# Performance work log

Measured on AMD Instinct MI355X. Metric: run time of the kernel, lower is better.

Reference implementation:

```python
import jax, jax.numpy as jnp
import numpy as np

EPS = 1e-5
HALT_THRESHOLD = 0.01
DILATIONS = (1, 2, 4)


def layer_norm(x, g, b):
    m = jnp.mean(x, axis=-1, keepdims=True)
    v = jnp.var(x, axis=-1, keepdims=True)
    return (x - m) * jax.lax.rsqrt(v + EPS) * g + b


def depthwise_conv(x, k, dilation):
    # x: [B,H,W,C], k: [kh,kw,1,C] (groups == C)
    pad = dilation * (k.shape[0] // 2)
    return jax.lax.conv_general_dilated(
        x, k, window_strides=(1, 1), padding=[(pad, pad), (pad, pad)],
        rhs_dilation=(dilation, dilation),
        dimension_numbers=('NHWC', 'HWIO', 'NHWC'),
        feature_group_count=x.shape[-1])


def setup_inputs() -> dict:
    key = jax.random.key(0)
    ks = jax.random.split(key, 12)
    B, H, W, C = 8, 96, 96, 64
    hid = 64
    P = C + len(DILATIONS) * C  # 256
    n = jax.random.normal
    return {
        'x': n(ks[0], (B, H, W, C), dtype=jnp.float32),
        'g1': jnp.ones((C,), jnp.float32), 'b1': jnp.zeros((C,), jnp.float32),
        'g2': jnp.ones((P,), jnp.float32), 'b2': jnp.zeros((P,), jnp.float32),
        'k1': 0.2 * n(ks[1], (3, 3, 1, C), dtype=jnp.float32),
        'k2': 0.2 * n(ks[2], (3, 3, 1, C), dtype=jnp.float32),
        'k3': 0.2 * n(ks[3], (3, 3, 1, C), dtype=jnp.float32),
        'Wu1': n(ks[4], (P, 2 * hid), dtype=jnp.float32) / np.sqrt(P),
        'bu1': jnp.zeros((2 * hid,), jnp.float32),
        'Wu2': n(ks[5], (2 * hid, hid), dtype=jnp.float32) / np.sqrt(2 * hid),
        'bu2': jnp.zeros((hid,), jnp.float32),
        'Wu3': n(ks[6], (hid, C), dtype=jnp.float32) / np.sqrt(hid),
        'bu3': jnp.zeros((C,), jnp.float32),
        'gh': jnp.ones((C,), jnp.float32), 'bh': jnp.zeros((C,), jnp.float32),
        'Wh1': n(ks[7], (C, hid), dtype=jnp.float32) / np.sqrt(C),
        'bh1': jnp.zeros((hid,), jnp.float32),
        'Wh2': n(ks[8], (hid, 1), dtype=jnp.float32) / np.sqrt(hid),
        'bh2': jnp.zeros((1,), jnp.float32),
        'max_steps': 8, 'min_steps': 1,
    }


def reference(x, g1, b1, g2, b2, k1, k2, k3, Wu1, bu1, Wu2, bu2, Wu3, bu3,
              gh, bh, Wh1, bh1, Wh2, bh2, max_steps, min_steps):
    gelu = lambda t: jax.nn.gelu(t, approximate=False)

    def forward_step(xs):
        # halt unit: LN -> Linear -> GELU -> Linear -> sigmoid
        h = gelu(layer_norm(xs, gh, bh) @ Wh1 + bh1)
        halt_probs = jax.nn.sigmoid(h @ Wh2 + bh2)[..., 0]  # [B,H,W]
        xn = layer_norm(xs, g1, b1)
        ps = [depthwise_conv(xn, k, d) for k, d in zip((k1, k2, k3), DILATIONS)]
        u = layer_norm(jnp.concatenate([xn] + ps, axis=-1), g2, b2)
        h1 = gelu(u @ Wu1 + bu1)
        h2 = gelu(h1 @ Wu2 + bu2)
        delta = h2 @ Wu3 + bu3
        return delta, halt_probs

    B, H, W, C = x.shape
    halted0 = jnp.zeros((B, H, W), jnp.bool_)
    acc0 = jnp.zeros((B, H, W), x.dtype)
    so0 = jnp.zeros_like(x)
    pc0 = jnp.zeros((B, H, W), x.dtype)

    def body(carry, step):
        xs, halted, acc, so, pc = carry
        delta, hp = forward_step(xs)
        active = ~halted
        af = active.astype(xs.dtype)
        xs = xs + delta * af[..., None]
        in_halt_phase = step >= (min_steps - 1)
        acc_n = acc + hp * af
        should_halt = (acc_n > 1.0 - HALT_THRESHOLD) & active
        halt_w = jnp.where(should_halt, 1.0 - (acc_n - hp), hp * af)
        so_n = so + xs * halt_w[..., None]
        halted_n = halted | should_halt
        acc = jnp.where(in_halt_phase, acc_n, acc)
        so = jnp.where(in_halt_phase, so_n, so)
        halted = jnp.where(in_halt_phase, halted_n, halted)
        pc = pc + jnp.where(in_halt_phase, af, jnp.ones_like(pc))
        return (xs, halted, acc, so, pc), None

    (xf, halted, acc, so, pc), _ = jax.lax.scan(
        body, (x, halted0, acc0, so0, pc0), jnp.arange(max_steps))
    # distribute remaining probability mass to cells that never halted
    remaining_w = (~halted).astype(x.dtype) * (1.0 - acc)
    so = so + xf * remaining_w[..., None]
    pc = pc / max_steps
    return so, halted, pc
```

## Files before the change

kernel.cpp:

```cpp
#include <hip/hip_runtime.h>
#include <hip/hip_bf16.h>

#define NPIX 73728
#define CH 64
#define HH 96
#define WW 96
#define PP 256

typedef __attribute__((ext_vector_type(8))) short short8;
typedef __attribute__((ext_vector_type(4))) float f32x4;

__device__ __forceinline__ float wsum64(float v) {
#pragma unroll
  for (int off = 32; off > 0; off >>= 1) v += __shfl_xor(v, off, 64);
  return v;
}
__device__ __forceinline__ float wsum16(float v) {
#pragma unroll
  for (int off = 1; off < 16; off <<= 1) v += __shfl_xor(v, off, 64);
  return v;
}
__device__ __forceinline__ float gelu_f(float x) {
  return 0.5f * x * (1.0f + erff(x * 0.70710678118654752f));
}
__device__ __forceinline__ float b2f(ushort u) {
  union { unsigned int i; float f; } c;
  c.i = ((unsigned int)u) << 16;
  return c.f;
}
__device__ __forceinline__ ushort f2b(float f) {
  union { float f; unsigned int i; } c;
  c.f = f;
  unsigned int r = c.i + 0x7fff + ((c.i >> 16) & 1);
  return (ushort)(r >> 16);
}

__global__ __launch_bounds__(256) void k_init(const float* __restrict__ x,
                                              float* __restrict__ xs,
                                              float* __restrict__ out,
                                              float* __restrict__ accb,
                                              float* __restrict__ xnf,
                                              int* __restrict__ cnt) {
  int i = blockIdx.x * 256 + threadIdx.x;
  if (i < NPIX * CH) xs[i] = x[i];
  if (i < NPIX * 66) out[i] = 0.0f;
  if (i < NPIX) { accb[i] = 0.0f; xnf[i] = 0.0f; }
  if (i < 8) cnt[i] = 0;
}

__global__ __launch_bounds__(256) void k_wprep(const float* __restrict__ W,
                                               ushort* __restrict__ Wp, int K,
                                               int N) {
  int t = blockIdx.x * 256 + threadIdx.x;
  if (t >= K * N) return;
  int j = t & 7, l = (t >> 3) & 63, tile = t >> 9;
  int NT = N >> 4;
  int kt = tile / NT, nt = tile - kt * NT;
  int k = kt * 32 + ((l >> 4) & 3) * 8 + j;
  int n = nt * 16 + (l & 15);
  Wp[t] = f2b(W[k * N + n]);
}

__global__ __launch_bounds__(256) void k_compact(const float* __restrict__ halted,
                                                 int* __restrict__ cnt,
                                                 int* __restrict__ idx, int step) {
  int p = blockIdx.x * 256 + threadIdx.x;
  bool active = (halted[p] == 0.0f);
  unsigned long long mask = __ballot(active);
  int lane = threadIdx.x & 63;
  int cw = __popcll(mask);
  int wbase = 0;
  if (lane == 0 && cw) wbase = atomicAdd(&cnt[step], cw);
  wbase = __shfl(wbase, 0, 64);
  if (active) {
    int off = __popcll(mask & ((1ull << lane) - 1ull));
    idx[wbase + off] = p;
  }
}

__global__ __launch_bounds__(256) void k_ln_halt(
    const float* __restrict__ xs, ushort* __restrict__ xn, float* __restrict__ hp,
    const float* __restrict__ halted, float* __restrict__ xnf,
    const float* __restrict__ g1, const float* __restrict__ b1,
    const float* __restrict__ gh, const float* __restrict__ bh,
    const float* __restrict__ Wh1, const float* __restrict__ bh1,
    const float* __restrict__ Wh2, const float* __restrict__ bh2) {
  __shared__ float lnbuf[4][64];
  __shared__ float partials[4][4][64];
  __shared__ int actf[4];
  int wave = threadIdx.x >> 6, lane = threadIdx.x & 63;
  int pix = blockIdx.x * 4 + wave;
  float hf = halted[pix];
  bool act = !(hf != 0.0f && xnf[pix] != 0.0f);
  if (lane == 0) actf[wave] = act ? 1 : 0;
  if (act) {
    float x = xs[(size_t)pix * CH + lane];
    float mean = wsum64(x) * (1.0f / 64.0f);
    float d = x - mean;
    float var = wsum64(d * d) * (1.0f / 64.0f);
    float rstd = rsqrtf(var + 1e-5f);
    float nrm = d * rstd;
    xn[(size_t)pix * CH + lane] = f2b(nrm * g1[lane] + b1[lane]);
    lnbuf[wave][lane] = nrm * gh[lane] + bh[lane];
    if (lane == 0) xnf[pix] = hf;
  } else {
    lnbuf[wave][lane] = 0.0f;
  }
  __syncthreads();
  if (!(actf[0] | actf[1] | actf[2] | actf[3])) return;

  float start = (wave == 0) ? bh1[lane] : 0.0f;
  float p0 = start, p1 = start, p2 = start, p3 = start;
  int i0 = wave * 16;
#pragma unroll 4
  for (int i = i0; i < i0 + 16; ++i) {
    float w = Wh1[i * 64 + lane];
    p0 = fmaf(lnbuf[0][i], w, p0);
    p1 = fmaf(lnbuf[1][i], w, p1);
    p2 = fmaf(lnbuf[2][i], w, p2);
    p3 = fmaf(lnbuf[3][i], w, p3);
  }
  partials[wave][0][lane] = p0;
  partials[wave][1][lane] = p1;
  partials[wave][2][lane] = p2;
  partials[wave][3][lane] = p3;
  __syncthreads();

  if (actf[wave]) {
    float s = (partials[0][wave][lane] + partials[1][wave][lane]) +
              (partials[2][wave][lane] + partials[3][wave][lane]);
    float acc = gelu_f(s);
    float c = wsum64(acc * Wh2[lane]);
    if (lane == 0) hp[pix] = 1.0f / (1.0f + expf(-(c + bh2[0])));
  }
}

template <bool EDGE>
__device__ __forceinline__ void do_taps(const ushort* pb,
                                        const float* __restrict__ k1,
                                        const float* __restrict__ k2,
                                        const float* __restrict__ k3, int cg,
                                        int y, int xq, float (&br)[4][4]) {
#pragma unroll
  for (int t = 0; t < 3; ++t) {
    const int dl = (t == 0) ? 1 : ((t == 1) ? 2 : 4);
    const float* kk = (t == 0) ? k1 : ((t == 1) ? k2 : k3);
    float a0 = 0.f, a1 = 0.f, a2 = 0.f, a3 = 0.f;
#pragma unroll
    for (int ky = 0; ky < 3; ++ky) {
#pragma unroll
      for (int kx = 0; kx < 3; ++kx) {
        const int dy = (ky - 1) * dl, dx = (kx - 1) * dl;
        if (EDGE && !(ky == 1 && kx == 1)) {
          if ((unsigned)(y + dy) >= HH) continue;
        }
        const float4 w = *(const float4*)&kk[(ky * 3 + kx) * CH + cg * 4];
        float v0, v1, v2, v3;
        if (ky == 1 && kx == 1) {
          v0 = br[0][0]; v1 = br[0][1]; v2 = br[0][2]; v3 = br[0][3];
        } else {
          ushort4 d4 = *(const ushort4*)(pb + (dy * WW + dx) * CH);
          v0 = b2f(d4.x); v1 = b2f(d4.y); v2 = b2f(d4.z); v3 = b2f(d4.w);
          if (EDGE && (unsigned)(xq + dx) >= WW) {
            v0 = 0.f; v1 = 0.f; v2 = 0.f; v3 = 0.f;
          }
        }
        a0 = fmaf(v0, w.x, a0); a1 = fmaf(v1, w.y, a1);
        a2 = fmaf(v2, w.z, a2); a3 = fmaf(v3, w.w, a3);
      }
    }
    br[t + 1][0] = a0; br[t + 1][1] = a1;
    br[t + 1][2] = a2; br[t + 1][3] = a3;
  }
}

__global__ __launch_bounds__(256) void k_conv_u(
    const ushort* __restrict__ xn, ushort* __restrict__ u,
    const int* __restrict__ idx, const int* __restrict__ cnt, int step,
    const float* __restrict__ k1, const float* __restrict__ k2,
    const float* __restrict__ k3, const float* __restrict__ g2,
    const float* __restrict__ b2) {
  int n = cnt[step];
  if (blockIdx.x * 16 >= n) return;
  int wv = threadIdx.x >> 6, l = threadIdx.x & 63;
  int cpx = l >> 4, cg = l & 15;
  int slot = blockIdx.x * 16 + wv * 4 + cpx;
  bool live = slot < n;
  int pix = idx[live ? slot : (n - 1)];
  int b = pix / (HH * WW);
  int rem = pix - b * (HH * WW);
  int y = rem / WW, xq = rem - (rem / WW) * WW;
  const ushort* pb = xn + (size_t)pix * CH + cg * 4;

  float br[4][4];
  {
    ushort4 c4 = *(const ushort4*)pb;
    br[0][0] = b2f(c4.x); br[0][1] = b2f(c4.y);
    br[0][2] = b2f(c4.z); br[0][3] = b2f(c4.w);
  }
  bool interior = (xq >= 4) && (xq <= WW - 5) && (y >= 4) && (y <= HH - 5);
  if (__all(interior))
    do_taps<false>(pb, k1, k2, k3, cg, y, xq, br);
  else
    do_taps<true>(pb, k1, k2, k3, cg, y, xq, br);

  float s = 0.f;
#pragma unroll
  for (int t = 0; t < 4; ++t)
#pragma unroll
    for (int c = 0; c < 4; ++c) s += br[t][c];
  float mean = wsum16(s) * (1.0f / 256.0f);
  float vs = 0.f;
#pragma unroll
  for (int t = 0; t < 4; ++t)
#pragma unroll
    for (int c = 0; c < 4; ++c) {
      float d = br[t][c] - mean;
      vs += d * d;
    }
  float rstd = rsqrtf(wsum16(vs) * (1.0f / 256.0f) + 1e-5f);
  ushort* ub = u + (size_t)blockIdx.x * 4096;
  int lr16 = wv * 4 + cpx;
  if (live) {
#pragma unroll
    for (int t = 0; t < 4; ++t) {
      float4 g = *(const float4*)&g2[t * CH + cg * 4];
      float4 bb = *(const float4*)&b2[t * CH + cg * 4];
      ushort4 o;
      o.x = f2b((br[t][0] - mean) * rstd * g.x + bb.x);
      o.y = f2b((br[t][1] - mean) * rstd * g.y + bb.y);
      o.z = f2b((br[t][2] - mean) * rstd * g.z + bb.z);
      o.w = f2b((br[t][3] - mean) * rstd * g.w + bb.w);
      int k0 = t * 64 + cg * 4;
      int kt = k0 >> 5, lg = (k0 >> 3) & 3, jj = k0 & 7;
      *(ushort4*)(ub + kt * 512 + (lg * 16 + lr16) * 8 + jj) = o;
    }
  }
}

__global__ __launch_bounds__(64) void k_mlp(
    const ushort* __restrict__ u, const int* __restrict__ idx,
    const int* __restrict__ cnt, int step, const ushort* __restrict__ Wp1,
    const ushort* __restrict__ Wp2, const ushort* __restrict__ Wp3,
    const float* __restrict__ bu1, const float* __restrict__ bu2,
    const float* __restrict__ bu3, const float* __restrict__ hp,
    float* __restrict__ xs, float* __restrict__ so, float* __restrict__ halted,
    float* __restrict__ accb, float* __restrict__ pc,
    const int* __restrict__ min_steps) {
  int n = cnt[step];
  if (blockIdx.x * 16 >= n) return;
  __shared__ ushort h1s[16 * 136];
  __shared__ ushort h2s[16 * 72];
  int l = threadIdx.x;
  int lr = l & 15, lg = l >> 4;
  const f32x4 vzero = {0.0f, 0.0f, 0.0f, 0.0f};

  int msteps = min_steps[0];
  bool in_halt = (step >= msteps - 1);
  int px = l >> 2, q = l & 3;
  int slotp = blockIdx.x * 16 + px;
  bool livep = slotp < n;
  int p = idx[livep ? slotp : (n - 1)];
  size_t base = (size_t)p * CH + q * 16;
  float4 xv[4], sv[4];
#pragma unroll
  for (int j = 0; j < 4; ++j) xv[j] = *(const float4*)&xs[base + j * 4];
  if (in_halt) {
#pragma unroll
    for (int j = 0; j < 4; ++j) sv[j] = *(const float4*)&so[base + j * 4];
  }
  float hpv = hp[p];
  float accv = accb[p];

  const ushort* ub = u + (size_t)blockIdx.x * 4096 + l * 8;
  short8 a[8];
#pragma unroll
  for (int kt = 0; kt < 8; ++kt) a[kt] = *(const short8*)(ub + kt * 512);
  f32x4 acc1[8];
#pragma unroll
  for (int nt = 0; nt < 8; ++nt) acc1[nt] = vzero;
#pragma unroll
  for (int kt = 0; kt < 8; ++kt) {
#pragma unroll
    for (int nt = 0; nt < 8; ++nt) {
      short8 b = *(const short8*)(Wp1 + ((kt * 8 + nt) * 64 + l) * 8);
      acc1[nt] = __builtin_amdgcn_mfma_f32_16x16x32_bf16(a[kt], b, acc1[nt], 0, 0, 0);
    }
  }
  ushort* h1w = h1s;
#pragma unroll
  for (int nt = 0; nt < 8; ++nt) {
    float bb = bu1[nt * 16 + lr];
#pragma unroll
    for (int i = 0; i < 4; ++i)
      h1w[(lg * 4 + i) * 136 + nt * 16 + lr] = f2b(gelu_f(acc1[nt][i] + bb));
  }

  f32x4 acc2[4];
#pragma unroll
  for (int nt = 0; nt < 4; ++nt) acc2[nt] = vzero;
#pragma unroll
  for (int kt = 0; kt < 4; ++kt) {
    short8 av = *(const short8*)(h1w + lr * 136 + kt * 32 + lg * 8);
#pragma unroll
    for (int nt = 0; nt < 4; ++nt) {
      short8 b = *(const short8*)(Wp2 + ((kt * 4 + nt) * 64 + l) * 8);
      acc2[nt] = __builtin_amdgcn_mfma_f32_16x16x32_bf16(av, b, acc2[nt], 0, 0, 0);
    }
  }
  ushort* h2w = h2s;
#pragma unroll
  for (int nt = 0; nt < 4; ++nt) {
    float bb = bu2[nt * 16 + lr];
#pragma unroll
    for (int i = 0; i < 4; ++i)
      h2w[(lg * 4 + i) * 72 + nt * 16 + lr] = f2b(gelu_f(acc2[nt][i] + bb));
  }

  f32x4 acc3[4];
#pragma unroll
  for (int nt = 0; nt < 4; ++nt) acc3[nt] = vzero;
#pragma unroll
  for (int kt = 0; kt < 2; ++kt) {
    short8 av = *(const short8*)(h2w + lr * 72 + kt * 32 + lg * 8);
#pragma unroll
    for (int nt = 0; nt < 4; ++nt) {
      short8 b = *(const short8*)(Wp3 + ((kt * 4 + nt) * 64 + l) * 8);
      acc3[nt] = __builtin_amdgcn_mfma_f32_16x16x32_bf16(av, b, acc3[nt], 0, 0, 0);
    }
  }
  float* df = (float*)h1w;
#pragma unroll
  for (int nt = 0; nt < 4; ++nt) {
    float bb = bu3[nt * 16 + lr];
#pragma unroll
    for (int i = 0; i < 4; ++i)
      df[(lg * 4 + i) * 68 + nt * 16 + lr] = acc3[nt][i] + bb;
  }

  if (livep) {
    float acc_n = accv + hpv;
    bool should_halt = (acc_n > 0.99f);
    float halt_w = should_halt ? (1.0f - (acc_n - hpv)) : hpv;
#pragma unroll
    for (int j = 0; j < 4; ++j) {
      float4 dv = *(const float4*)&df[px * 68 + q * 16 + j * 4];
      float4 x2 = xv[j];
      x2.x += dv.x; x2.y += dv.y; x2.z += dv.z; x2.w += dv.w;
      *(float4*)&xs[base + j * 4] = x2;
      if (in_halt) {
        float4 s2 = sv[j];
        s2.x += x2.x * halt_w;
        s2.y += x2.y * halt_w;
        s2.z += x2.z * halt_w;
        s2.w += x2.w * halt_w;
        *(float4*)&so[base + j * 4] = s2;
      }
    }
    if (q == 0) {
      if (in_halt) {
        accb[p] = acc_n;
        halted[p] = should_halt ? 1.0f : 0.0f;
      }
      pc[p] += 1.0f;
    }
  }
}

__global__ __launch_bounds__(256) void k_final(
    const float* __restrict__ xs, float* __restrict__ so,
    const float* __restrict__ halted, const float* __restrict__ accb,
    float* __restrict__ pc, const int* __restrict__ max_steps) {
  int wave = threadIdx.x >> 6, lane = threadIdx.x & 63;
  int pix = blockIdx.x * 4 + wave;
  float rem = (halted[pix] == 0.0f) ? (1.0f - accb[pix]) : 0.0f;
  so[(size_t)pix * CH + lane] += xs[(size_t)pix * CH + lane] * rem;
  if (lane == 0) pc[pix] *= 1.0f / (float)max_steps[0];
}

extern "C" void kernel_launch(void* const* d_in, const int* in_sizes, int n_in,
                              void* d_out, int out_size, void* d_ws,
                              size_t ws_size, hipStream_t stream) {
  const float* x   = (const float*)d_in[0];
  const float* g1  = (const float*)d_in[1];
  const float* b1  = (const float*)d_in[2];
  const float* g2  = (const float*)d_in[3];
  const float* b2  = (const float*)d_in[4];
  const float* k1  = (const float*)d_in[5];
  const float* k2  = (const float*)d_in[6];
  const float* k3  = (const float*)d_in[7];
  const float* Wu1 = (const float*)d_in[8];
  const float* bu1 = (const float*)d_in[9];
  const float* Wu2 = (const float*)d_in[10];
  const float* bu2 = (const float*)d_in[11];
  const float* Wu3 = (const float*)d_in[12];
  const float* bu3 = (const float*)d_in[13];
  const float* gh  = (const float*)d_in[14];
  const float* bh  = (const float*)d_in[15];
  const float* Wh1 = (const float*)d_in[16];
  const float* bh1 = (const float*)d_in[17];
  const float* Wh2 = (const float*)d_in[18];
  const float* bh2 = (const float*)d_in[19];
  const int* max_steps = (const int*)d_in[20];
  const int* min_steps = (const int*)d_in[21];

  if (ws_size < (size_t)68000000) return;
  char* ws = (char*)d_ws;
  float*  xs   = (float*)(ws);
  ushort* xn   = (ushort*)(ws + 18874368);
  ushort* u    = (ushort*)(ws + 28311552);
  float*  hp   = (float*)(ws + 66060288);
  float*  accb = (float*)(ws + 66355200);
  ushort* Wp1  = (ushort*)(ws + 66650112);
  ushort* Wp2  = (ushort*)(ws + 66715648);
  ushort* Wp3  = (ushort*)(ws + 66732032);
  float*  xnf  = (float*)(ws + 66740224);
  int*    idx  = (int*)(ws + 67035136);
  int*    cnt  = (int*)(ws + 67330048);
  float* so = (float*)d_out;
  float* halted = so + (size_t)NPIX * CH;
  float* pc = halted + NPIX;

  k_wprep<<<128, 256, 0, stream>>>(Wu1, Wp1, 256, 128);
  k_wprep<<<32, 256, 0, stream>>>(Wu2, Wp2, 128, 64);
  k_wprep<<<16, 256, 0, stream>>>(Wu3, Wp3, 64, 64);
  k_init<<<19008, 256, 0, stream>>>(x, xs, so, accb, xnf, cnt);
  for (int step = 0; step < 8; ++step) {
    k_compact<<<NPIX / 256, 256, 0, stream>>>(halted, cnt, idx, step);
    k_ln_halt<<<NPIX / 4, 256, 0, stream>>>(xs, xn, hp, halted, xnf, g1, b1,
                                            gh, bh, Wh1, bh1, Wh2, bh2);
    k_conv_u<<<NPIX / 16, 256, 0, stream>>>(xn, u, idx, cnt, step, k1, k2, k3,
                                            g2, b2);
    k_mlp<<<NPIX / 16, 64, 0, stream>>>(u, idx, cnt, step, Wp1, Wp2, Wp3, bu1,
                                        bu2, bu3, hp, xs, so, halted, accb, pc,
                                        min_steps);
  }
  k_final<<<NPIX / 4, 256, 0, stream>>>(xs, so, halted, accb, pc, max_steps);
}
```

Before: 694.1 us.

## Fuse depthwise conv and LayerNorm into the MLP kernel via an LDS slab

Removes the separate conv+LN kernel and computes the dilated depthwise convolutions and the 256-channel LayerNorm inside the MLP kernel. The result goes straight into a shared-memory slab in MFMA operand layout instead of a global `u` buffer. This drops a large global write and read of the bf16 intermediate, plus one launch per step. In exchange, each 64-thread block now does the conv work serially over four iterations instead of using four waves, which lengthens per-block latency and raises register and LDS use.

```diff
diff --git a/kernel.cpp b/kernel.cpp
--- a/kernel.cpp
+++ b/kernel.cpp
@@ -174,81 +174,21 @@
   }
 }
 
-__global__ __launch_bounds__(256) void k_conv_u(
-    const ushort* __restrict__ xn, ushort* __restrict__ u,
-    const int* __restrict__ idx, const int* __restrict__ cnt, int step,
-    const float* __restrict__ k1, const float* __restrict__ k2,
-    const float* __restrict__ k3, const float* __restrict__ g2,
-    const float* __restrict__ b2) {
-  int n = cnt[step];
-  if (blockIdx.x * 16 >= n) return;
-  int wv = threadIdx.x >> 6, l = threadIdx.x & 63;
-  int cpx = l >> 4, cg = l & 15;
-  int slot = blockIdx.x * 16 + wv * 4 + cpx;
-  bool live = slot < n;
-  int pix = idx[live ? slot : (n - 1)];
-  int b = pix / (HH * WW);
-  int rem = pix - b * (HH * WW);
-  int y = rem / WW, xq = rem - (rem / WW) * WW;
-  const ushort* pb = xn + (size_t)pix * CH + cg * 4;
-
-  float br[4][4];
-  {
-    ushort4 c4 = *(const ushort4*)pb;
-    br[0][0] = b2f(c4.x); br[0][1] = b2f(c4.y);
-    br[0][2] = b2f(c4.z); br[0][3] = b2f(c4.w);
-  }
-  bool interior = (xq >= 4) && (xq <= WW - 5) && (y >= 4) && (y <= HH - 5);
-  if (__all(interior))
-    do_taps<false>(pb, k1, k2, k3, cg, y, xq, br);
-  else
-    do_taps<true>(pb, k1, k2, k3, cg, y, xq, br);
-
-  float s = 0.f;
-#pragma unroll
-  for (int t = 0; t < 4; ++t)
-#pragma unroll
-    for (int c = 0; c < 4; ++c) s += br[t][c];
-  float mean = wsum16(s) * (1.0f / 256.0f);
-  float vs = 0.f;
-#pragma unroll
-  for (int t = 0; t < 4; ++t)
-#pragma unroll
-    for (int c = 0; c < 4; ++c) {
-      float d = br[t][c] - mean;
-      vs += d * d;
-    }
-  float rstd = rsqrtf(wsum16(vs) * (1.0f / 256.0f) + 1e-5f);
-  ushort* ub = u + (size_t)blockIdx.x * 4096;
-  int lr16 = wv * 4 + cpx;
-  if (live) {
-#pragma unroll
-    for (int t = 0; t < 4; ++t) {
-      float4 g = *(const float4*)&g2[t * CH + cg * 4];
-      float4 bb = *(const float4*)&b2[t * CH + cg * 4];
-      ushort4 o;
-      o.x = f2b((br[t][0] - mean) * rstd * g.x + bb.x);
-      o.y = f2b((br[t][1] - mean) * rstd * g.y + bb.y);
-      o.z = f2b((br[t][2] - mean) * rstd * g.z + bb.z);
-      o.w = f2b((br[t][3] - mean) * rstd * g.w + bb.w);
-      int k0 = t * 64 + cg * 4;
-      int kt = k0 >> 5, lg = (k0 >> 3) & 3, jj = k0 & 7;
-      *(ushort4*)(ub + kt * 512 + (lg * 16 + lr16) * 8 + jj) = o;
-    }
-  }
-}
-
 __global__ __launch_bounds__(64) void k_mlp(
-    const ushort* __restrict__ u, const int* __restrict__ idx,
-    const int* __restrict__ cnt, int step, const ushort* __restrict__ Wp1,
-    const ushort* __restrict__ Wp2, const ushort* __restrict__ Wp3,
-    const float* __restrict__ bu1, const float* __restrict__ bu2,
-    const float* __restrict__ bu3, const float* __restrict__ hp,
-    float* __restrict__ xs, float* __restrict__ so, float* __restrict__ halted,
+    const ushort* __restrict__ xn, const int* __restrict__ idx,
+    const int* __restrict__ cnt, int step, const float* __restrict__ k1,
+    const float* __restrict__ k2, const float* __restrict__ k3,
+    const float* __restrict__ g2, const float* __restrict__ b2,
+    const ushort* __restrict__ Wp1, const ushort* __restrict__ Wp2,
+    const ushort* __restrict__ Wp3, const float* __restrict__ bu1,
+    const float* __restrict__ bu2, const float* __restrict__ bu3,
+    const float* __restrict__ hp, float* __restrict__ xs,
+    float* __restrict__ so, float* __restrict__ halted,
     float* __restrict__ accb, float* __restrict__ pc,
     const int* __restrict__ min_steps) {
   int n = cnt[step];
   if (blockIdx.x * 16 >= n) return;
+  __shared__ ushort uslab[4096];
   __shared__ ushort h1s[16 * 136];
   __shared__ ushort h2s[16 * 72];
   int l = threadIdx.x;
@@ -272,10 +212,67 @@
   float hpv = hp[p];
   float accv = accb[p];
 
-  const ushort* ub = u + (size_t)blockIdx.x * 4096 + l * 8;
+  {
+    int cpx = l >> 4, cg = l & 15;
+#pragma unroll
+    for (int it = 0; it < 4; ++it) {
+      int slot = blockIdx.x * 16 + it * 4 + cpx;
+      bool live = slot < n;
+      int pix = idx[live ? slot : (n - 1)];
+      int b = pix / (HH * WW);
+      int rem = pix - b * (HH * WW);
+      int y = rem / WW, xq = rem - (rem / WW) * WW;
+      const ushort* pb = xn + (size_t)pix * CH + cg * 4;
+      float br[4][4];
+      {
+        ushort4 c4 = *(const ushort4*)pb;
+        br[0][0] = b2f(c4.x); br[0][1] = b2f(c4.y);
+        br[0][2] = b2f(c4.z); br[0][3] = b2f(c4.w);
+      }
+      bool interior = (xq >= 4) && (xq <= WW - 5) && (y >= 4) && (y <= HH - 5);
+      if (__all(interior))
+        do_taps<false>(pb, k1, k2, k3, cg, y, xq, br);
+      else
+        do_taps<true>(pb, k1, k2, k3, cg, y, xq, br);
+
+      float s = 0.f;
+#pragma unroll
+      for (int t = 0; t < 4; ++t)
+#pragma unroll
+        for (int c = 0; c < 4; ++c) s += br[t][c];
+      float mean = wsum16(s) * (1.0f / 256.0f);
+      float vs = 0.f;
+#pragma unroll
+      for (int t = 0; t < 4; ++t)
+#pragma unroll
+        for (int c = 0; c < 4; ++c) {
+          float d = br[t][c] - mean;
+          vs += d * d;
+        }
+      float rstd = rsqrtf(wsum16(vs) * (1.0f / 256.0f) + 1e-5f);
+      int lr16 = it * 4 + cpx;
+      if (live) {
+#pragma unroll
+        for (int t = 0; t < 4; ++t) {
+          float4 g = *(const float4*)&g2[t * CH + cg * 4];
+          float4 bb = *(const float4*)&b2[t * CH + cg * 4];
+          ushort4 o;
+          o.x = f2b((br[t][0] - mean) * rstd * g.x + bb.x);
+          o.y = f2b((br[t][1] - mean) * rstd * g.y + bb.y);
+          o.z = f2b((br[t][2] - mean) * rstd * g.z + bb.z);
+          o.w = f2b((br[t][3] - mean) * rstd * g.w + bb.w);
+          int k0 = t * 64 + cg * 4;
+          int kt = k0 >> 5, lg2 = (k0 >> 3) & 3, jj = k0 & 7;
+          *(ushort4*)(uslab + kt * 512 + (lg2 * 16 + lr16) * 8 + jj) = o;
+        }
+      }
+    }
+  }
+
   short8 a[8];
 #pragma unroll
-  for (int kt = 0; kt < 8; ++kt) a[kt] = *(const short8*)(ub + kt * 512);
+  for (int kt = 0; kt < 8; ++kt)
+    a[kt] = *(const short8*)(uslab + kt * 512 + l * 8);
   f32x4 acc1[8];
 #pragma unroll
   for (int nt = 0; nt < 8; ++nt) acc1[nt] = vzero;
@@ -408,7 +405,6 @@
   char* ws = (char*)d_ws;
   float*  xs   = (float*)(ws);
   ushort* xn   = (ushort*)(ws + 18874368);
-  ushort* u    = (ushort*)(ws + 28311552);
   float*  hp   = (float*)(ws + 66060288);
   float*  accb = (float*)(ws + 66355200);
   ushort* Wp1  = (ushort*)(ws + 66650112);
@@ -429,11 +425,9 @@
     k_compact<<<NPIX / 256, 256, 0, stream>>>(halted, cnt, idx, step);
     k_ln_halt<<<NPIX / 4, 256, 0, stream>>>(xs, xn, hp, halted, xnf, g1, b1,
                                             gh, bh, Wh1, bh1, Wh2, bh2);
-    k_conv_u<<<NPIX / 16, 256, 0, stream>>>(xn, u, idx, cnt, step, k1, k2, k3,
-                                            g2, b2);
-    k_mlp<<<NPIX / 16, 64, 0, stream>>>(u, idx, cnt, step, Wp1, Wp2, Wp3, bu1,
-                                        bu2, bu3, hp, xs, so, halted, accb, pc,
-                                        min_steps);
+    k_mlp<<<NPIX / 16, 64, 0, stream>>>(xn, idx, cnt, step, k1, k2, k3, g2, b2,
+                                        Wp1, Wp2, Wp3, bu1, bu2, bu3, hp, xs,
+                                        so, halted, accb, pc, min_steps);
   }
   k_final<<<NPIX / 4, 256, 0, stream>>>(xs, so, halted, accb, pc, max_steps);
 }
```

Result: slower. 841.3 us (+21.2%).

## Fuse active-pixel compaction into MLP kernel and drive LN/halt from compacted lists

Applied to the files above, without the earlier changes.

Removes the separate per-step compaction kernel. The MLP epilogue now appends still-active pixels to the next step's index list through a wave ballot and an atomic. The LN/halt kernel now iterates over a compacted list (the previous step's list, which still covers pixels that halted on the last step and need xn for the conv halo) instead of launching over every pixel and checking the halted and xnf flags. This saves one launch per step and the full-grid scans, but it needs per-step index storage and changes the order of pixel indices from sequential to atomic-driven, which can hurt memory locality.

```diff
diff --git a/kernel.cpp b/kernel.cpp
--- a/kernel.cpp
+++ b/kernel.cpp
@@ -39,13 +39,13 @@
                                               float* __restrict__ xs,
                                               float* __restrict__ out,
                                               float* __restrict__ accb,
-                                              float* __restrict__ xnf,
+                                              int* __restrict__ idx,
                                               int* __restrict__ cnt) {
   int i = blockIdx.x * 256 + threadIdx.x;
   if (i < NPIX * CH) xs[i] = x[i];
   if (i < NPIX * 66) out[i] = 0.0f;
-  if (i < NPIX) { accb[i] = 0.0f; xnf[i] = 0.0f; }
-  if (i < 8) cnt[i] = 0;
+  if (i < NPIX) { accb[i] = 0.0f; idx[i] = i; }
+  if (i < 9) cnt[i] = (i == 0) ? NPIX : 0;
 }
 
 __global__ __launch_bounds__(256) void k_wprep(const float* __restrict__ W,
@@ -61,38 +61,21 @@
   Wp[t] = f2b(W[k * N + n]);
 }
 
-__global__ __launch_bounds__(256) void k_compact(const float* __restrict__ halted,
-                                                 int* __restrict__ cnt,
-                                                 int* __restrict__ idx, int step) {
-  int p = blockIdx.x * 256 + threadIdx.x;
-  bool active = (halted[p] == 0.0f);
-  unsigned long long mask = __ballot(active);
-  int lane = threadIdx.x & 63;
-  int cw = __popcll(mask);
-  int wbase = 0;
-  if (lane == 0 && cw) wbase = atomicAdd(&cnt[step], cw);
-  wbase = __shfl(wbase, 0, 64);
-  if (active) {
-    int off = __popcll(mask & ((1ull << lane) - 1ull));
-    idx[wbase + off] = p;
-  }
-}
-
 __global__ __launch_bounds__(256) void k_ln_halt(
     const float* __restrict__ xs, ushort* __restrict__ xn, float* __restrict__ hp,
-    const float* __restrict__ halted, float* __restrict__ xnf,
+    const int* __restrict__ lst, const int* __restrict__ cnt, int lslot,
     const float* __restrict__ g1, const float* __restrict__ b1,
     const float* __restrict__ gh, const float* __restrict__ bh,
     const float* __restrict__ Wh1, const float* __restrict__ bh1,
     const float* __restrict__ Wh2, const float* __restrict__ bh2) {
+  int m = cnt[lslot];
+  if (blockIdx.x * 4 >= m) return;
   __shared__ float lnbuf[4][64];
   __shared__ float partials[4][4][64];
-  __shared__ int actf[4];
   int wave = threadIdx.x >> 6, lane = threadIdx.x & 63;
-  int pix = blockIdx.x * 4 + wave;
-  float hf = halted[pix];
-  bool act = !(hf != 0.0f && xnf[pix] != 0.0f);
-  if (lane == 0) actf[wave] = act ? 1 : 0;
+  int slot = blockIdx.x * 4 + wave;
+  bool act = slot < m;
+  int pix = lst[act ? slot : m - 1];
   if (act) {
     float x = xs[(size_t)pix * CH + lane];
     float mean = wsum64(x) * (1.0f / 64.0f);
@@ -102,12 +85,10 @@
     float nrm = d * rstd;
     xn[(size_t)pix * CH + lane] = f2b(nrm * g1[lane] + b1[lane]);
     lnbuf[wave][lane] = nrm * gh[lane] + bh[lane];
-    if (lane == 0) xnf[pix] = hf;
   } else {
     lnbuf[wave][lane] = 0.0f;
   }
   __syncthreads();
-  if (!(actf[0] | actf[1] | actf[2] | actf[3])) return;
 
   float start = (wave == 0) ? bh1[lane] : 0.0f;
   float p0 = start, p1 = start, p2 = start, p3 = start;
@@ -126,7 +107,7 @@
   partials[wave][3][lane] = p3;
   __syncthreads();
 
-  if (actf[wave]) {
+  if (act) {
     float s = (partials[0][wave][lane] + partials[1][wave][lane]) +
               (partials[2][wave][lane] + partials[3][wave][lane]);
     float acc = gelu_f(s);
@@ -176,7 +157,7 @@
 
 __global__ __launch_bounds__(256) void k_conv_u(
     const ushort* __restrict__ xn, ushort* __restrict__ u,
-    const int* __restrict__ idx, const int* __restrict__ cnt, int step,
+    const int* __restrict__ lst, const int* __restrict__ cnt, int step,
     const float* __restrict__ k1, const float* __restrict__ k2,
     const float* __restrict__ k3, const float* __restrict__ g2,
     const float* __restrict__ b2) {
@@ -186,7 +167,7 @@
   int cpx = l >> 4, cg = l & 15;
   int slot = blockIdx.x * 16 + wv * 4 + cpx;
   bool live = slot < n;
-  int pix = idx[live ? slot : (n - 1)];
+  int pix = lst[live ? slot : (n - 1)];
   int b = pix / (HH * WW);
   int rem = pix - b * (HH * WW);
   int y = rem / WW, xq = rem - (rem / WW) * WW;
@@ -239,12 +220,13 @@
 }
 
 __global__ __launch_bounds__(64) void k_mlp(
-    const ushort* __restrict__ u, const int* __restrict__ idx,
-    const int* __restrict__ cnt, int step, const ushort* __restrict__ Wp1,
-    const ushort* __restrict__ Wp2, const ushort* __restrict__ Wp3,
-    const float* __restrict__ bu1, const float* __restrict__ bu2,
-    const float* __restrict__ bu3, const float* __restrict__ hp,
-    float* __restrict__ xs, float* __restrict__ so, float* __restrict__ halted,
+    const ushort* __restrict__ u, const int* __restrict__ lst,
+    int* __restrict__ nxt, int* __restrict__ cnt, int step,
+    const ushort* __restrict__ Wp1, const ushort* __restrict__ Wp2,
+    const ushort* __restrict__ Wp3, const float* __restrict__ bu1,
+    const float* __restrict__ bu2, const float* __restrict__ bu3,
+    const float* __restrict__ hp, float* __restrict__ xs,
+    float* __restrict__ so, float* __restrict__ halted,
     float* __restrict__ accb, float* __restrict__ pc,
     const int* __restrict__ min_steps) {
   int n = cnt[step];
@@ -260,7 +242,7 @@
   int px = l >> 2, q = l & 3;
   int slotp = blockIdx.x * 16 + px;
   bool livep = slotp < n;
-  int p = idx[livep ? slotp : (n - 1)];
+  int p = lst[livep ? slotp : (n - 1)];
   size_t base = (size_t)p * CH + q * 16;
   float4 xv[4], sv[4];
 #pragma unroll
@@ -338,10 +320,10 @@
       df[(lg * 4 + i) * 68 + nt * 16 + lr] = acc3[nt][i] + bb;
   }
 
+  float acc_n = accv + hpv;
+  bool should_halt = in_halt && (acc_n > 0.99f);
   if (livep) {
-    float acc_n = accv + hpv;
-    bool should_halt = (acc_n > 0.99f);
-    float halt_w = should_halt ? (1.0f - (acc_n - hpv)) : hpv;
+    float halt_w = (acc_n > 0.99f) ? (1.0f - (acc_n - hpv)) : hpv;
 #pragma unroll
     for (int j = 0; j < 4; ++j) {
       float4 dv = *(const float4*)&df[px * 68 + q * 16 + j * 4];
@@ -364,6 +346,17 @@
       }
       pc[p] += 1.0f;
     }
+  }
+
+  bool keep = livep && !should_halt;
+  unsigned long long m_ = __ballot(q == 0 && keep);
+  int cw = __popcll(m_);
+  int wbase = 0;
+  if (l == 0 && cw) wbase = atomicAdd(&cnt[step + 1], cw);
+  wbase = __shfl(wbase, 0, 64);
+  if (q == 0 && keep) {
+    int off = __popcll(m_ & ((1ull << l) - 1ull));
+    nxt[wbase + off] = p;
   }
 }
 
@@ -404,7 +397,7 @@
   const int* max_steps = (const int*)d_in[20];
   const int* min_steps = (const int*)d_in[21];
 
-  if (ws_size < (size_t)68000000) return;
+  if (ws_size < (size_t)70000000) return;
   char* ws = (char*)d_ws;
   float*  xs   = (float*)(ws);
   ushort* xn   = (ushort*)(ws + 18874368);
@@ -414,9 +407,8 @@
   ushort* Wp1  = (ushort*)(ws + 66650112);
   ushort* Wp2  = (ushort*)(ws + 66715648);
   ushort* Wp3  = (ushort*)(ws + 66732032);
-  float*  xnf  = (float*)(ws + 66740224);
-  int*    idx  = (int*)(ws + 67035136);
-  int*    cnt  = (int*)(ws + 67330048);
+  int*    idx  = (int*)(ws + 66740224);
+  int*    cnt  = (int*)(ws + 69394432);
   float* so = (float*)d_out;
   float* halted = so + (size_t)NPIX * CH;
   float* pc = halted + NPIX;
@@ -424,16 +416,18 @@
   k_wprep<<<128, 256, 0, stream>>>(Wu1, Wp1, 256, 128);
   k_wprep<<<32, 256, 0, stream>>>(Wu2, Wp2, 128, 64);
   k_wprep<<<16, 256, 0, stream>>>(Wu3, Wp3, 64, 64);
-  k_init<<<19008, 256, 0, stream>>>(x, xs, so, accb, xnf, cnt);
+  k_init<<<19008, 256, 0, stream>>>(x, xs, so, accb, idx, cnt);
   for (int step = 0; step < 8; ++step) {
-    k_compact<<<NPIX / 256, 256, 0, stream>>>(halted, cnt, idx, step);
-    k_ln_halt<<<NPIX / 4, 256, 0, stream>>>(xs, xn, hp, halted, xnf, g1, b1,
-                                            gh, bh, Wh1, bh1, Wh2, bh2);
-    k_conv_u<<<NPIX / 16, 256, 0, stream>>>(xn, u, idx, cnt, step, k1, k2, k3,
-                                            g2, b2);
-    k_mlp<<<NPIX / 16, 64, 0, stream>>>(u, idx, cnt, step, Wp1, Wp2, Wp3, bu1,
-                                        bu2, bu3, hp, xs, so, halted, accb, pc,
-                                        min_steps);
+    int ls = (step == 0) ? 0 : (step - 1);
+    k_ln_halt<<<NPIX / 4, 256, 0, stream>>>(xs, xn, hp, idx + (size_t)ls * NPIX,
+                                            cnt, ls, g1, b1, gh, bh, Wh1, bh1,
+                                            Wh2, bh2);
+    k_conv_u<<<NPIX / 16, 256, 0, stream>>>(xn, u, idx + (size_t)step * NPIX,
+                                            cnt, step, k1, k2, k3, g2, b2);
+    k_mlp<<<NPIX / 16, 64, 0, stream>>>(u, idx + (size_t)step * NPIX,
+                                        idx + (size_t)(step + 1) * NPIX, cnt,
+                                        step, Wp1, Wp2, Wp3, bu1, bu2, bu3, hp,
+                                        xs, so, halted, accb, pc, min_steps);
   }
   k_final<<<NPIX / 4, 256, 0, stream>>>(xs, so, halted, accb, pc, max_steps);
 }
```

New measurement: 664.2 us. 1.05x faster.
